# Kernel tuning notes

Hardware: AMD Instinct MI355X
Metric: run time of the kernel (lower is better)

The kernel has to match this reference:

```python
import jax, jax.numpy as jnp
import numpy as np

# sym8 decomposition low-pass filter (pywt convention, 16 taps)
SYM8_DEC_LO = np.array([
    -0.0033824159510061256, -0.0005421323317911481, 0.03169508781149298,
    0.007607487324917605, -0.1432942383508097, -0.061273359067658524,
    0.4813596512583722, 0.7771857517005235, 0.3644418948353314,
    -0.05194583810770904, -0.027219029917056003, 0.049137179673607506,
    0.003808752013890615, -0.01495225833704823, -0.0003029205147213668,
    0.0018899503327594609], dtype=np.float64)

MAX_LEV = 8
POWER = 2.0
EPS = 1e-12


def _filters():
    dec_lo = jnp.asarray(SYM8_DEC_LO, dtype=jnp.float32)
    n = dec_lo.shape[0]
    alt = jnp.where(jnp.arange(n) % 2 == 0, 1.0, -1.0).astype(jnp.float32)
    dec_hi = alt * dec_lo[::-1]  # quadrature mirror filter
    # conv_general_dilated is cross-correlation (like torch conv1d in ptwt),
    # so flip the decomposition filters.
    return jnp.stack([dec_lo[::-1], dec_hi[::-1]])[:, None, :]  # [2,1,F] OIW


def _dwt_step(x, filt):
    # x: [N, L] -> [2N, L_out]; per node the (approx, detail) pair is interleaved,
    # which yields pywt 'natural' packet order after repeated application.
    F = filt.shape[-1]
    L = x.shape[1]
    padl = (2 * F - 3) // 2            # ptwt _fwt_pad, reflect mode
    padr = padl + (L % 2)              # extra right pad for odd lengths
    xp = jnp.pad(x, ((0, 0), (padl, padr)), mode='reflect')
    y = jax.lax.conv_general_dilated(
        xp[:, None, :], filt, window_strides=(2,), padding='VALID')  # [N,2,L']
    return y.reshape(-1, y.shape[-1])


def reference(pt_data):
    B = pt_data.shape[0]
    filt = _filters()
    x = pt_data
    for _ in range(MAX_LEV):           # fixed, small tree depth (8 levels)
        x = _dwt_step(x, filt)
    wp = x.reshape(B, 2 ** MAX_LEV, -1)         # [B, 256, L_final] natural order
    wp_log = jnp.log(jnp.abs(wp) ** POWER + EPS)
    # torch: stack(dim=-1) -> [B, L, P]; unsqueeze(1); permute(0,1,3,2) -> [B,1,P,L]
    return wp_log[:, None]             # [B, 1, 256, L_final]


def setup_inputs() -> dict:
    key = jax.random.key(0)
    pt_data = jax.random.normal(key, (128, 65536), dtype=jnp.float32)
    return {"pt_data": pt_data}
```

## Files before the change

kernel.cpp:

```cpp
#include <hip/hip_runtime.h>


#define BT 512

__device__ __constant__ float FL[16] = {
     0.0018899503327594609f, -0.0003029205147213668f, -0.01495225833704823f,
     0.003808752013890615f,   0.049137179673607506f,  -0.027219029917056003f,
    -0.05194583810770904f,    0.3644418948353314f,     0.7771857517005235f,
     0.4813596512583722f,    -0.061273359067658524f,  -0.1432942383508097f,
     0.007607487324917605f,   0.03169508781149298f,   -0.0005421323317911481f,
    -0.0033824159510061256f
};
__device__ __constant__ float FH[16] = {
     0.0033824159510061256f, -0.0005421323317911481f, -0.03169508781149298f,
     0.007607487324917605f,   0.1432942383508097f,    -0.061273359067658524f,
    -0.4813596512583722f,     0.7771857517005235f,    -0.3644418948353314f,
    -0.05194583810770904f,    0.027219029917056003f,   0.049137179673607506f,
    -0.003808752013890615f,  -0.01495225833704823f,    0.0003029205147213668f,
     0.0018899503327594609f
};
__device__ __constant__ float FLE[8] = {
     0.0018899503327594609f, -0.01495225833704823f,  0.049137179673607506f,
    -0.05194583810770904f,   0.7771857517005235f,   -0.061273359067658524f,
     0.007607487324917605f, -0.0005421323317911481f };
__device__ __constant__ float FLO[8] = {
    -0.0003029205147213668f, 0.003808752013890615f, -0.027219029917056003f,
     0.3644418948353314f,    0.4813596512583722f,   -0.1432942383508097f,
     0.03169508781149298f,  -0.0033824159510061256f };
__device__ __constant__ float FHE[8] = {
     0.0033824159510061256f, -0.03169508781149298f,  0.1432942383508097f,
    -0.4813596512583722f,   -0.3644418948353314f,    0.027219029917056003f,
    -0.003808752013890615f,  0.0003029205147213668f };
__device__ __constant__ float FHO[8] = {
    -0.0005421323317911481f, 0.007607487324917605f, -0.061273359067658524f,
     0.7771857517005235f,   -0.05194583810770904f,   0.049137179673607506f,
    -0.01495225833704823f,   0.0018899503327594609f };

__device__ __forceinline__ int reflect(int q, int L) {
    q = (q < 0) ? -q : q;
    return (q >= L) ? (2 * L - 2 - q) : q;
}

__device__ __forceinline__ void gload_lds16(const float* g, float* l) {
    __builtin_amdgcn_global_load_lds(
        (const __attribute__((address_space(1))) void*)g,
        (__attribute__((address_space(3))) void*)l, 16, 0, 0);
}

__device__ __forceinline__ void load20(const float* __restrict__ lds, int base,
                                       float w[20]) {
#pragma unroll
    for (int k = 0; k < 5; ++k) {
        const float4 v = *reinterpret_cast<const float4*>(&lds[base + 4 * k]);
        w[4 * k] = v.x; w[4 * k + 1] = v.y; w[4 * k + 2] = v.z; w[4 * k + 3] = v.w;
    }
}

__device__ __forceinline__ void conv2(const float w[20], float& lo0, float& hi0,
                                      float& lo1, float& hi1) {
    lo0 = hi0 = lo1 = hi1 = 0.f;
#pragma unroll
    for (int t = 0; t < 16; ++t) {
        const float cl = FL[t], ch = FH[t];
        lo0 = fmaf(w[t], cl, lo0);
        hi0 = fmaf(w[t], ch, hi0);
        lo1 = fmaf(w[t + 2], cl, lo1);
        hi1 = fmaf(w[t + 2], ch, hi1);
    }
}

__device__ __forceinline__ void eo_put(float* __restrict__ E, float* __restrict__ O,
                                       int q, float v) {
    ((q & 1) ? O : E)[8 + (q >> 1)] = v;
}

template <int Pin, int Wout, int Sin, int Sout, int Lc>
__device__ __forceinline__ void f03_stage(const float* __restrict__ in,
                                          float* __restrict__ out, int o_lo) {
    constexpr int GPS = Wout / 2;
    for (int g = threadIdx.x; g < Pin * GPS; g += BT) {
        const int r = g / GPS;
        const int u = g - r * GPS;
        const int s0 = 2 * u;
        const int q0 = o_lo + s0;
        const float* pin = in + r * Sin;
        float lo0, hi0, lo1, hi1;
        if (q0 >= 0 && q0 + 2 <= Lc) {
            float w[20];
            load20(pin, 4 * u, w);
            conv2(w, lo0, hi0, lo1, hi1);
        } else {
#pragma unroll
            for (int e = 0; e < 2; ++e) {
                const int jr = reflect(q0 + e, Lc);
                const int rb = 2 * (jr - o_lo);
                float l = 0.f, h = 0.f;
#pragma unroll
                for (int t = 0; t < 16; ++t) {
                    const float v = pin[rb + t];
                    l = fmaf(v, FL[t], l);
                    h = fmaf(v, FH[t], h);
                }
                if (e == 0) { lo0 = l; hi0 = h; } else { lo1 = l; hi1 = h; }
            }
        }
        *reinterpret_cast<float2*>(&out[(2 * r) * Sout + s0])     = make_float2(lo0, lo1);
        *reinterpret_cast<float2*>(&out[(2 * r + 1) * Sout + s0]) = make_float2(hi0, hi1);
    }
}

__global__ __launch_bounds__(BT, 8) void dwt_f03(
    const float* __restrict__ x, float* __restrict__ y) {
    constexpr int M  = 258;
    constexpr int WX = 4338, SX = 4340;
    constexpr int W0 = 2162, S0 = 2164;
    constexpr int W1 = 1074, S1 = 1076;
    constexpr int W2 = 530,  S2 = 532;
    __shared__ __align__(16) float bufA[4340];
    __shared__ __align__(16) float bufB[4328];

    const int seg = blockIdx.x;
    const int n   = blockIdx.y;
    const int b0  = M * seg;
    const int a2  = 2 * b0 - 14;
    const int c1  = 4 * b0 - 42;
    const int a0  = 8 * b0 - 98;
    const int px0 = 16 * b0 - 210;
    const float* row = x + (size_t)n * 65536;

    if (px0 >= 0 && px0 + WX <= 65536) {
        const float2* rp = reinterpret_cast<const float2*>(row + px0);
        for (int h = threadIdx.x; h < WX / 2; h += BT)
            *reinterpret_cast<float2*>(&bufA[2 * h]) = rp[h];
    } else {
        for (int p = threadIdx.x; p < WX; p += BT)
            bufA[p] = row[reflect(px0 + p, 65536)];
    }
    __syncthreads();

    f03_stage<1, W0, SX, S0, 32775>(bufA, bufB, a0);
    __syncthreads();
    f03_stage<2, W1, S0, S1, 16395>(bufB, bufA, c1);
    __syncthreads();
    f03_stage<4, W2, S1, S2, 8205>(bufA, bufB, a2);
    __syncthreads();

    {
        constexpr int GPS = M / 2;
        float* yg = y + (size_t)(16 * n) * 4160;
        for (int g = threadIdx.x; g < 8 * GPS; g += BT) {
            const int r  = g / GPS;
            const int u  = g - r * GPS;
            const int j0 = b0 + 2 * u;
            if (j0 >= 4110) continue;
            float w[20];
            load20(bufB + r * S2, 4 * u, w);
            float lo0, hi0, lo1, hi1;
            conv2(w, lo0, hi0, lo1, hi1);
            float* Elo = yg + (size_t)(2 * r) * 4160;
            const int s = 8 + (j0 >> 1);
            Elo[s]          = lo0;
            Elo[2076 + s]   = lo1;
            Elo[4160 + s]   = hi0;
            Elo[6236 + s]   = hi1;
        }
    }
}

__device__ __forceinline__ void read12(const float* __restrict__ b, int w0,
                                       float* __restrict__ r) {
#pragma unroll
    for (int k = 0; k < 3; ++k) {
        const float4 v = *reinterpret_cast<const float4*>(&b[w0 + 4 * k]);
        r[4 * k] = v.x; r[4 * k + 1] = v.y; r[4 * k + 2] = v.z; r[4 * k + 3] = v.w;
    }
}

template <int OFF>
__device__ __forceinline__ void conv4eo(const float e[12], const float o[12],
                                        float lo[4], float hi[4]) {
#pragma unroll
    for (int d = 0; d < 4; ++d) { lo[d] = 0.f; hi[d] = 0.f; }
#pragma unroll
    for (int s = 0; s < 8; ++s) {
        const float fle = FLE[s], flo = FLO[s], fhe = FHE[s], fho = FHO[s];
#pragma unroll
        for (int d = 0; d < 4; ++d) {
            const float ev = e[OFF + d + s], ov = o[OFF + d + s];
            lo[d] = fmaf(ev, fle, lo[d]);
            lo[d] = fmaf(ov, flo, lo[d]);
            hi[d] = fmaf(ev, fhe, hi[d]);
            hi[d] = fmaf(ov, fho, hi[d]);
        }
    }
}

template <int Ls, int P, int Sin, int Sout, bool LOG>
__device__ __forceinline__ void stage_eo(const float* __restrict__ inb,
                                         float* __restrict__ outb,
                                         float* __restrict__ outg) {
    constexpr int H    = Ls / 2;
    constexpr int LOUT = H + 7;
    constexpr int GPS  = (LOUT + 3) / 4;
    constexpr int SEi  = Sin / 2;
    constexpr int SEo  = Sout / 2;
    for (int g = threadIdx.x; g < P * GPS; g += BT) {
        const int p  = g / GPS;
        const int u  = g - p * GPS;
        const int j0 = 4 * u;
        const float* Ei = inb + p * Sin;
        const float* Oi = Ei + SEi;
        float e[12], o[12];
        read12(Ei, 4 * u, e);
        read12(Oi, 4 * u, o);
        float lo[4], hi[4];
        conv4eo<1>(e, o, lo, hi);
        if (LOG) {
            float r0[4], r1[4];
#pragma unroll
            for (int d = 0; d < 4; ++d) {
                r0[d] = __logf(fmaf(lo[d], lo[d], 1e-12f));
                r1[d] = __logf(fmaf(hi[d], hi[d], 1e-12f));
            }
            float* y0 = outg + (2 * p) * 270 + j0;
            float* y1 = y0 + 270;
            if (j0 + 3 < 270) {
                *reinterpret_cast<float2*>(y0)     = make_float2(r0[0], r0[1]);
                *reinterpret_cast<float2*>(y0 + 2) = make_float2(r0[2], r0[3]);
                *reinterpret_cast<float2*>(y1)     = make_float2(r1[0], r1[1]);
                *reinterpret_cast<float2*>(y1 + 2) = make_float2(r1[2], r1[3]);
            } else {
                *reinterpret_cast<float2*>(y0) = make_float2(r0[0], r0[1]);
                *reinterpret_cast<float2*>(y1) = make_float2(r1[0], r1[1]);
            }
        } else {
            float* El = outb + (2 * p) * Sout;
            float* Ol = El + SEo;
            float* Eh = outb + (2 * p + 1) * Sout;
            float* Oh = Eh + SEo;
            if (j0 + 3 < LOUT) {
                *reinterpret_cast<float2*>(&El[8 + 2 * u]) = make_float2(lo[0], lo[2]);
                *reinterpret_cast<float2*>(&Ol[8 + 2 * u]) = make_float2(lo[1], lo[3]);
                *reinterpret_cast<float2*>(&Eh[8 + 2 * u]) = make_float2(hi[0], hi[2]);
                *reinterpret_cast<float2*>(&Oh[8 + 2 * u]) = make_float2(hi[1], hi[3]);
            } else {
#pragma unroll
                for (int d = 0; d < 4; ++d)
                    if (j0 + d < LOUT) {
                        eo_put(El, Ol, j0 + d, lo[d]);
                        eo_put(Eh, Oh, j0 + d, hi[d]);
                    }
            }
            if (j0 <= 14 || j0 >= LOUT - 18) {
#pragma unroll
                for (int d = 0; d < 4; ++d) {
                    const int j = j0 + d;
                    if (j >= 1 && j <= 14) {
                        eo_put(El, Ol, -j, lo[d]);
                        eo_put(Eh, Oh, -j, hi[d]);
                    }
                    if (j >= LOUT - 15 && j <= LOUT - 2) {
                        eo_put(El, Ol, 2 * LOUT - 2 - j, lo[d]);
                        eo_put(Eh, Oh, 2 * LOUT - 2 - j, hi[d]);
                    }
                }
            }
        }
    }
}

__global__ __launch_bounds__(BT, 8) void dwt_quad_eo(
    const float* __restrict__ x, float* __restrict__ y) {
    __shared__ __align__(16) float bufA[4352];
    __shared__ __align__(16) float bufB[4544];

    const int m = blockIdx.x;
    const float* row = x + (size_t)m * 4160;

    const int wave = threadIdx.x >> 6;
    const int lane = threadIdx.x & 63;
    for (int c = wave; c < 17; c += 8)
        gload_lds16(row + c * 256 + lane * 4, &bufA[c * 256]);
    __syncthreads();

    if (threadIdx.x < 28) {
        const int t = threadIdx.x;
        float* Ex = bufA;
        float* Ox = bufA + 2076;
        if (t < 7)       Ex[7 - t]          = Ex[9 + t];
        else if (t < 14) Ox[14 - t]         = Ox[t + 1];
        else if (t < 21) Ex[2063 + (t - 14)] = Ex[2062 - (t - 14)];
        else             Ox[2063 + (t - 21)] = Ox[2061 - (t - 21)];
    }
    __syncthreads();

    stage_eo<4110, 1, 4152, 2104, false>(bufA, bufB, nullptr);
    __syncthreads();
    stage_eo<2062, 2, 2104, 1080, false>(bufB, bufA, nullptr);
    __syncthreads();
    stage_eo<1038, 4, 1080, 568, false>(bufA, bufB, nullptr);
    __syncthreads();
    stage_eo<526, 8, 568, 0, true>(bufB, nullptr, y + (size_t)m * 4320);
}

extern "C" void kernel_launch(void* const* d_in, const int* in_sizes, int n_in,
                              void* d_out, int out_size, void* d_ws, size_t ws_size,
                              hipStream_t stream) {
    const float* in = (const float*)d_in[0];
    float* out = (float*)d_out;
    float* wsB = (float*)d_ws;
    (void)ws_size; (void)out_size; (void)n_in; (void)in_sizes;

    { dim3 g(16, 128); dwt_f03<<<g, BT, 0, stream>>>(in, wsB); }
    dwt_quad_eo<<<2048, BT, 0, stream>>>(wsB, out);
}
```

Before: 76.72 us.

## Use even/odd split LDS layout and 4-output conv in first DWT kernel

The first fused kernel now deinterleaves the input row into even and odd planes in LDS. Its three inner stages and the final stage use the polyphase 4-output convolution (conv4eo) already used by the second kernel. This cuts LDS reads and register window loads per output and reuses each loaded window across more outputs. The segment size changes from 258 to 260 to match the 4-wide grouping, and the LDS buffers grow slightly. The boundary path falls back to per-output reflected scalar convolutions.

```diff
diff --git a/kernel.cpp b/kernel.cpp
--- a/kernel.cpp
+++ b/kernel.cpp
@@ -47,25 +47,45 @@
         (__attribute__((address_space(3))) void*)l, 16, 0, 0);
 }
 
-__device__ __forceinline__ void load20(const float* __restrict__ lds, int base,
-                                       float w[20]) {
-#pragma unroll
-    for (int k = 0; k < 5; ++k) {
-        const float4 v = *reinterpret_cast<const float4*>(&lds[base + 4 * k]);
-        w[4 * k] = v.x; w[4 * k + 1] = v.y; w[4 * k + 2] = v.z; w[4 * k + 3] = v.w;
-    }
-}
-
-__device__ __forceinline__ void conv2(const float w[20], float& lo0, float& hi0,
-                                      float& lo1, float& hi1) {
-    lo0 = hi0 = lo1 = hi1 = 0.f;
-#pragma unroll
-    for (int t = 0; t < 16; ++t) {
-        const float cl = FL[t], ch = FH[t];
-        lo0 = fmaf(w[t], cl, lo0);
-        hi0 = fmaf(w[t], ch, hi0);
-        lo1 = fmaf(w[t + 2], cl, lo1);
-        hi1 = fmaf(w[t + 2], ch, hi1);
+__device__ __forceinline__ void read12(const float* __restrict__ b, int w0,
+                                       float* __restrict__ r) {
+#pragma unroll
+    for (int k = 0; k < 3; ++k) {
+        const float4 v = *reinterpret_cast<const float4*>(&b[w0 + 4 * k]);
+        r[4 * k] = v.x; r[4 * k + 1] = v.y; r[4 * k + 2] = v.z; r[4 * k + 3] = v.w;
+    }
+}
+
+template <int OFF>
+__device__ __forceinline__ void conv4eo(const float e[12], const float o[12],
+                                        float lo[4], float hi[4]) {
+#pragma unroll
+    for (int d = 0; d < 4; ++d) { lo[d] = 0.f; hi[d] = 0.f; }
+#pragma unroll
+    for (int s = 0; s < 8; ++s) {
+        const float fle = FLE[s], flo = FLO[s], fhe = FHE[s], fho = FHO[s];
+#pragma unroll
+        for (int d = 0; d < 4; ++d) {
+            const float ev = e[OFF + d + s], ov = o[OFF + d + s];
+            lo[d] = fmaf(ev, fle, lo[d]);
+            lo[d] = fmaf(ov, flo, lo[d]);
+            hi[d] = fmaf(ev, fhe, hi[d]);
+            hi[d] = fmaf(ov, fho, hi[d]);
+        }
+    }
+}
+
+__device__ __forceinline__ void conv1s(const float* __restrict__ E,
+                                       const float* __restrict__ O,
+                                       int s, float& lo, float& hi) {
+    lo = hi = 0.f;
+#pragma unroll
+    for (int k = 0; k < 8; ++k) {
+        const float ev = E[s + k], ov = O[s + k];
+        lo = fmaf(ev, FLE[k], lo);
+        lo = fmaf(ov, FLO[k], lo);
+        hi = fmaf(ev, FHE[k], hi);
+        hi = fmaf(ov, FHO[k], hi);
     }
 }
 
@@ -74,51 +94,46 @@
     ((q & 1) ? O : E)[8 + (q >> 1)] = v;
 }
 
-template <int Pin, int Wout, int Sin, int Sout, int Lc>
-__device__ __forceinline__ void f03_stage(const float* __restrict__ in,
-                                          float* __restrict__ out, int o_lo) {
-    constexpr int GPS = Wout / 2;
-    for (int g = threadIdx.x; g < Pin * GPS; g += BT) {
-        const int r = g / GPS;
-        const int u = g - r * GPS;
-        const int s0 = 2 * u;
+template <int Pin, int NV, int SEp, int SEc, int Lc>
+__device__ __forceinline__ void f03_stage_eo(const float* __restrict__ inb,
+                                             float* __restrict__ outb, int o_lo) {
+    for (int g = threadIdx.x; g < Pin * NV; g += BT) {
+        const int r = g / NV;
+        const int v = g - r * NV;
+        const int s0 = 4 * v;
         const int q0 = o_lo + s0;
-        const float* pin = in + r * Sin;
-        float lo0, hi0, lo1, hi1;
-        if (q0 >= 0 && q0 + 2 <= Lc) {
-            float w[20];
-            load20(pin, 4 * u, w);
-            conv2(w, lo0, hi0, lo1, hi1);
+        const float* PE = inb + r * (2 * SEp);
+        const float* PO = PE + SEp;
+        float lo[4], hi[4];
+        if (q0 >= 0 && q0 + 4 <= Lc) {
+            float e[12], o[12];
+            read12(PE, 4 * v, e);
+            read12(PO, 4 * v, o);
+            conv4eo<0>(e, o, lo, hi);
         } else {
 #pragma unroll
-            for (int e = 0; e < 2; ++e) {
-                const int jr = reflect(q0 + e, Lc);
-                const int rb = 2 * (jr - o_lo);
-                float l = 0.f, h = 0.f;
-#pragma unroll
-                for (int t = 0; t < 16; ++t) {
-                    const float v = pin[rb + t];
-                    l = fmaf(v, FL[t], l);
-                    h = fmaf(v, FH[t], h);
-                }
-                if (e == 0) { lo0 = l; hi0 = h; } else { lo1 = l; hi1 = h; }
-            }
-        }
-        *reinterpret_cast<float2*>(&out[(2 * r) * Sout + s0])     = make_float2(lo0, lo1);
-        *reinterpret_cast<float2*>(&out[(2 * r + 1) * Sout + s0]) = make_float2(hi0, hi1);
+            for (int d = 0; d < 4; ++d) {
+                const int jr = reflect(q0 + d, Lc);
+                conv1s(PE, PO, jr - o_lo, lo[d], hi[d]);
+            }
+        }
+        float* CEl = outb + (2 * r) * (2 * SEc);
+        float* COl = CEl + SEc;
+        float* CEh = outb + (2 * r + 1) * (2 * SEc);
+        float* COh = CEh + SEc;
+        *reinterpret_cast<float2*>(&CEl[2 * v]) = make_float2(lo[0], lo[2]);
+        *reinterpret_cast<float2*>(&COl[2 * v]) = make_float2(lo[1], lo[3]);
+        *reinterpret_cast<float2*>(&CEh[2 * v]) = make_float2(hi[0], hi[2]);
+        *reinterpret_cast<float2*>(&COh[2 * v]) = make_float2(hi[1], hi[3]);
     }
 }
 
 __global__ __launch_bounds__(BT, 8) void dwt_f03(
     const float* __restrict__ x, float* __restrict__ y) {
-    constexpr int M  = 258;
-    constexpr int WX = 4338, SX = 4340;
-    constexpr int W0 = 2162, S0 = 2164;
-    constexpr int W1 = 1074, S1 = 1076;
-    constexpr int W2 = 530,  S2 = 532;
-    __shared__ __align__(16) float bufA[4340];
-    __shared__ __align__(16) float bufB[4328];
-
+    __shared__ __align__(16) float bufA[4400];
+    __shared__ __align__(16) float bufB[4384];
+
+    constexpr int M = 260;
     const int seg = blockIdx.x;
     const int n   = blockIdx.y;
     const int b0  = M * seg;
@@ -128,69 +143,58 @@
     const int px0 = 16 * b0 - 210;
     const float* row = x + (size_t)n * 65536;
 
-    if (px0 >= 0 && px0 + WX <= 65536) {
+    float* XE = bufA;
+    float* XO = bufA + 2200;
+    if (px0 >= 0 && px0 + 4400 <= 65536) {
         const float2* rp = reinterpret_cast<const float2*>(row + px0);
-        for (int h = threadIdx.x; h < WX / 2; h += BT)
-            *reinterpret_cast<float2*>(&bufA[2 * h]) = rp[h];
+        for (int i = threadIdx.x; i < 2200; i += BT) {
+            const float2 v = rp[i];
+            XE[i] = v.x; XO[i] = v.y;
+        }
     } else {
-        for (int p = threadIdx.x; p < WX; p += BT)
-            bufA[p] = row[reflect(px0 + p, 65536)];
-    }
-    __syncthreads();
-
-    f03_stage<1, W0, SX, S0, 32775>(bufA, bufB, a0);
-    __syncthreads();
-    f03_stage<2, W1, S0, S1, 16395>(bufB, bufA, c1);
-    __syncthreads();
-    f03_stage<4, W2, S1, S2, 8205>(bufA, bufB, a2);
+        for (int i = threadIdx.x; i < 2200; i += BT) {
+            XE[i] = row[reflect(px0 + 2 * i, 65536)];
+            XO[i] = row[reflect(px0 + 2 * i + 1, 65536)];
+        }
+    }
+    __syncthreads();
+
+    f03_stage_eo<1, 548, 2200, 1096, 32775>(bufA, bufB, a0);
+    __syncthreads();
+    f03_stage_eo<2, 272, 1096, 544, 16395>(bufB, bufA, c1);
+    __syncthreads();
+    f03_stage_eo<4, 134, 544, 268, 8205>(bufA, bufB, a2);
     __syncthreads();
 
     {
-        constexpr int GPS = M / 2;
+        constexpr int NVF = 65;
         float* yg = y + (size_t)(16 * n) * 4160;
-        for (int g = threadIdx.x; g < 8 * GPS; g += BT) {
-            const int r  = g / GPS;
-            const int u  = g - r * GPS;
-            const int j0 = b0 + 2 * u;
+        for (int g = threadIdx.x; g < 8 * NVF; g += BT) {
+            const int r  = g / NVF;
+            const int v  = g - r * NVF;
+            const int j0 = b0 + 4 * v;
             if (j0 >= 4110) continue;
-            float w[20];
-            load20(bufB + r * S2, 4 * u, w);
-            float lo0, hi0, lo1, hi1;
-            conv2(w, lo0, hi0, lo1, hi1);
+            const float* PE = bufB + r * (2 * 268);
+            const float* PO = PE + 268;
+            float e[12], o[12];
+            read12(PE, 4 * v, e);
+            read12(PO, 4 * v, o);
+            float lo[4], hi[4];
+            conv4eo<0>(e, o, lo, hi);
             float* Elo = yg + (size_t)(2 * r) * 4160;
+            float* Olo = Elo + 2076;
+            float* Ehi = Elo + 4160;
+            float* Ohi = Ehi + 2076;
             const int s = 8 + (j0 >> 1);
-            Elo[s]          = lo0;
-            Elo[2076 + s]   = lo1;
-            Elo[4160 + s]   = hi0;
-            Elo[6236 + s]   = hi1;
-        }
-    }
-}
-
-__device__ __forceinline__ void read12(const float* __restrict__ b, int w0,
-                                       float* __restrict__ r) {
-#pragma unroll
-    for (int k = 0; k < 3; ++k) {
-        const float4 v = *reinterpret_cast<const float4*>(&b[w0 + 4 * k]);
-        r[4 * k] = v.x; r[4 * k + 1] = v.y; r[4 * k + 2] = v.z; r[4 * k + 3] = v.w;
-    }
-}
-
-template <int OFF>
-__device__ __forceinline__ void conv4eo(const float e[12], const float o[12],
-                                        float lo[4], float hi[4]) {
-#pragma unroll
-    for (int d = 0; d < 4; ++d) { lo[d] = 0.f; hi[d] = 0.f; }
-#pragma unroll
-    for (int s = 0; s < 8; ++s) {
-        const float fle = FLE[s], flo = FLO[s], fhe = FHE[s], fho = FHO[s];
-#pragma unroll
-        for (int d = 0; d < 4; ++d) {
-            const float ev = e[OFF + d + s], ov = o[OFF + d + s];
-            lo[d] = fmaf(ev, fle, lo[d]);
-            lo[d] = fmaf(ov, flo, lo[d]);
-            hi[d] = fmaf(ev, fhe, hi[d]);
-            hi[d] = fmaf(ov, fho, hi[d]);
+            if (j0 + 4 <= 4110) {
+                *reinterpret_cast<float2*>(&Elo[s]) = make_float2(lo[0], lo[2]);
+                *reinterpret_cast<float2*>(&Olo[s]) = make_float2(lo[1], lo[3]);
+                *reinterpret_cast<float2*>(&Ehi[s]) = make_float2(hi[0], hi[2]);
+                *reinterpret_cast<float2*>(&Ohi[s]) = make_float2(hi[1], hi[3]);
+            } else {
+                Elo[s] = lo[0]; Olo[s] = lo[1];
+                Ehi[s] = hi[0]; Ohi[s] = hi[1];
+            }
         }
     }
 }
@@ -287,8 +291,8 @@
         const int t = threadIdx.x;
         float* Ex = bufA;
         float* Ox = bufA + 2076;
-        if (t < 7)       Ex[7 - t]          = Ex[9 + t];
-        else if (t < 14) Ox[14 - t]         = Ox[t + 1];
+        if (t < 7)       Ex[7 - t]           = Ex[9 + t];
+        else if (t < 14) Ox[14 - t]          = Ox[t + 1];
         else if (t < 21) Ex[2063 + (t - 14)] = Ex[2062 - (t - 14)];
         else             Ox[2063 + (t - 21)] = Ox[2061 - (t - 21)];
     }
```

Measured after the change: 98.97 us. 29.0% more time.
